# Kernel optimization log

Hardware: AMD Instinct MI355X
Metric: run time of the kernel (lower is better)

## Reference

```python
import jax, jax.numpy as jnp
import numpy as np


def setup_inputs() -> dict:
    key = jax.random.key(0)
    k1, k2, k3, k4 = jax.random.split(key, 4)
    B, D_IN, D, N, A = 32, 2048, 128, 400000, 7
    return {
        "x": jax.random.normal(k1, (B, D_IN), dtype=jnp.float32),
        "W_enc": jax.random.normal(k2, (D_IN, D), dtype=jnp.float32) * 0.02,
        "b_enc": jnp.zeros((D,), dtype=jnp.float32),
        "reps": jax.random.normal(k3, (N, D), dtype=jnp.float32),
        "actions": jax.random.normal(k4, (N, A), dtype=jnp.float32),
        "k": 5,
    }


def reference(x, W_enc, b_enc, reps, actions, k):
    # encoder embed: [B, D]
    batch_rep = x @ W_enc + b_enc
    # euclidean cdist: [B, N]
    sq = (
        jnp.sum(batch_rep * batch_rep, axis=-1, keepdims=True)
        + jnp.sum(reps * reps, axis=-1)[None, :]
        - 2.0 * (batch_rep @ reps.T)
    )
    dists = jnp.sqrt(jnp.maximum(sq, 1e-12))
    # top-k smallest distances
    neg_topk, indices = jax.lax.top_k(-dists, k)  # [B, k]
    top_k_distances = -neg_topk
    # gather actions: [B, k, A]
    top_k_actions = actions[indices]
    # softmax(-distance) weights: [B, k]
    weights = jax.nn.softmax(-top_k_distances, axis=1)
    # weighted average: [B, A]
    pred = jnp.sum(top_k_actions * weights[..., None], axis=1)
    return pred
```

## Files before the change

kernel.cpp:

```cpp
#include <hip/hip_runtime.h>
#include <math.h>

#define BATCH 32
#define DIN   2048
#define DK    128
#define NREPS 400000
#define ACT   7
#define NGRP  (NREPS / 64)

__device__ __forceinline__ void topk_insert(float s, int n,
    float& d0, float& d1, float& d2, float& d3, float& d4,
    int& i0, int& i1, int& i2, int& i3, int& i4)
{
    if (s < d4) {
        if (s < d3) {
            d4 = d3; i4 = i3;
            if (s < d2) {
                d3 = d2; i3 = i2;
                if (s < d1) {
                    d2 = d1; i2 = i1;
                    if (s < d0) { d1 = d0; i1 = i0; d0 = s; i0 = n; }
                    else        { d1 = s;  i1 = n; }
                } else { d2 = s; i2 = n; }
            } else { d3 = s; i3 = n; }
        } else { d4 = s; i4 = n; }
    }
}

__global__ __launch_bounds__(256) void encoder_kernel(
    const float* __restrict__ x, const float* __restrict__ W,
    const float* __restrict__ be, float* __restrict__ brept,
    float* __restrict__ brnorm)
{
    __shared__ float xs[DIN];
    __shared__ float part[256];
    __shared__ float vrow[DK];
    const int b = blockIdx.x, t = threadIdx.x;

    const float4* x4 = (const float4*)(x + (size_t)b * DIN);
    float4* xs4 = (float4*)xs;
    xs4[t]       = x4[t];
    xs4[t + 256] = x4[t + 256];
    __syncthreads();

    const int d = t & 127, h = t >> 7;
    const float* Wp = W + (size_t)(h * 1024) * DK + d;
    const float* xp = xs + h * 1024;
    float a0 = 0.f, a1 = 0.f, a2 = 0.f, a3 = 0.f;
    for (int i = 0; i < 1024; i += 4) {
        a0 = fmaf(xp[i],     Wp[(size_t)i * DK],       a0);
        a1 = fmaf(xp[i + 1], Wp[(size_t)(i + 1) * DK], a1);
        a2 = fmaf(xp[i + 2], Wp[(size_t)(i + 2) * DK], a2);
        a3 = fmaf(xp[i + 3], Wp[(size_t)(i + 3) * DK], a3);
    }
    part[t] = (a0 + a1) + (a2 + a3);
    __syncthreads();
    if (t < DK) {
        float v = part[t] + part[t + 128] + be[t];
        brept[t * BATCH + b] = -2.0f * v;
        vrow[t] = v * v;
    }
    __syncthreads();
    if (t == 0) {
        float s = 0.f;
        for (int i = 0; i < DK; i++) s += vrow[i];
        brnorm[b] = s;
    }
}

__global__ __launch_bounds__(256, 4) void dist_topk_kernel(
    const float* __restrict__ reps, const float* __restrict__ brt,
    float* __restrict__ pd, int* __restrict__ pi, int nwaves)
{
    __shared__ float wdist[4 * 64 * 36];
    const int t = threadIdx.x, g = blockIdx.x;
    const int wid = t >> 6, ln = t & 63;
    const int b = ln & 31, h = ln >> 5;
    float* wd = wdist + wid * (64 * 36);

    float d0 = 3.0e38f, d1 = 3.0e38f, d2 = 3.0e38f, d3 = 3.0e38f, d4 = 3.0e38f;
    int   i0 = 0, i1 = 0, i2 = 0, i3 = 0, i4 = 0;

    for (int grp = g * 4 + wid; grp < NGRP; grp += nwaves) {
        const float4* rp = (const float4*)(reps + (size_t)(grp * 64 + ln) * DK);
        float acc[32];
        #pragma unroll
        for (int i = 0; i < 32; i++) acc[i] = 0.f;
        float nrm = 0.f;

        #pragma unroll 1
        for (int c = 0; c < 4; c++) {
            float4 r[8];
            #pragma unroll
            for (int q = 0; q < 8; q++) r[q] = rp[c * 8 + q];
            const float* bp0 = brt + c * 32 * BATCH;
            #pragma unroll
            for (int q = 0; q < 8; q++) {
                const float4 rr = r[q];
                nrm = fmaf(rr.x, rr.x, nrm);
                nrm = fmaf(rr.y, rr.y, nrm);
                nrm = fmaf(rr.z, rr.z, nrm);
                nrm = fmaf(rr.w, rr.w, nrm);
                const float* bp = bp0 + q * 4 * BATCH;
                #pragma unroll
                for (int bb = 0; bb < 32; bb++) {
                    float a = acc[bb];
                    a = fmaf(bp[bb],             rr.x, a);
                    a = fmaf(bp[BATCH + bb],     rr.y, a);
                    a = fmaf(bp[2 * BATCH + bb], rr.z, a);
                    a = fmaf(bp[3 * BATCH + bb], rr.w, a);
                    acc[bb] = a;
                }
            }
        }

        #pragma unroll
        for (int q = 0; q < 8; q++) {
            float4 v;
            v.x = acc[4 * q]     + nrm;
            v.y = acc[4 * q + 1] + nrm;
            v.z = acc[4 * q + 2] + nrm;
            v.w = acc[4 * q + 3] + nrm;
            *(float4*)&wd[ln * 36 + 4 * q] = v;
        }
        asm volatile("s_waitcnt lgkmcnt(0)" ::: "memory");

        const int nb = grp * 64;
        #pragma unroll 4
        for (int s = 0; s < 32; s++) {
            const int row = h * 32 + s;
            const float dv = wd[row * 36 + b];
            topk_insert(dv, nb + row, d0, d1, d2, d3, d4, i0, i1, i2, i3, i4);
        }
        asm volatile("s_waitcnt lgkmcnt(0)" ::: "memory");
    }

    __syncthreads();
    float* cD = wdist;
    int*   cI = (int*)(wdist + 1280);
    {
        const int base = t * 5;
        cD[base]     = d0; cI[base]     = i0;
        cD[base + 1] = d1; cI[base + 1] = i1;
        cD[base + 2] = d2; cI[base + 2] = i2;
        cD[base + 3] = d3; cI[base + 3] = i3;
        cD[base + 4] = d4; cI[base + 4] = i4;
    }
    __syncthreads();
    if (t < 32) {
        float e0 = 3.0e38f, e1 = 3.0e38f, e2 = 3.0e38f, e3 = 3.0e38f, e4 = 3.0e38f;
        int   j0 = 0, j1 = 0, j2 = 0, j3 = 0, j4 = 0;
        for (int j = 0; j < 8; j++) {
            const int base = (t + 32 * j) * 5;
            #pragma unroll
            for (int e = 0; e < 5; e++)
                topk_insert(cD[base + e], cI[base + e],
                            e0, e1, e2, e3, e4, j0, j1, j2, j3, j4);
        }
        const int ob = (g * BATCH + t) * 5;
        pd[ob] = e0; pd[ob + 1] = e1; pd[ob + 2] = e2; pd[ob + 3] = e3; pd[ob + 4] = e4;
        pi[ob] = j0; pi[ob + 1] = j1; pi[ob + 2] = j2; pi[ob + 3] = j3; pi[ob + 4] = j4;
    }
}

__global__ __launch_bounds__(256) void final_kernel(
    const float* __restrict__ pd, const int* __restrict__ pi,
    const float* __restrict__ brnorm, const float* __restrict__ actions,
    float* __restrict__ out, int G)
{
    __shared__ float lD[256 * 5];
    __shared__ int   lI[256 * 5];
    __shared__ float sD[32 * 5];
    __shared__ int   sI[32 * 5];
    const int b = blockIdx.x, t = threadIdx.x;

    float d0 = 3.0e38f, d1 = 3.0e38f, d2 = 3.0e38f, d3 = 3.0e38f, d4 = 3.0e38f;
    int   i0 = 0, i1 = 0, i2 = 0, i3 = 0, i4 = 0;
    for (int g = t; g < G; g += 256) {
        const int base = (g * BATCH + b) * 5;
        #pragma unroll
        for (int e = 0; e < 5; e++)
            topk_insert(pd[base + e], pi[base + e],
                        d0, d1, d2, d3, d4, i0, i1, i2, i3, i4);
    }
    lD[t * 5] = d0; lD[t * 5 + 1] = d1; lD[t * 5 + 2] = d2; lD[t * 5 + 3] = d3; lD[t * 5 + 4] = d4;
    lI[t * 5] = i0; lI[t * 5 + 1] = i1; lI[t * 5 + 2] = i2; lI[t * 5 + 3] = i3; lI[t * 5 + 4] = i4;
    __syncthreads();
    if (t < 32) {
        d0 = d1 = d2 = d3 = d4 = 3.0e38f; i0 = i1 = i2 = i3 = i4 = 0;
        for (int s = 0; s < 8; s++) {
            const int base = (t * 8 + s) * 5;
            #pragma unroll
            for (int e = 0; e < 5; e++)
                topk_insert(lD[base + e], lI[base + e],
                            d0, d1, d2, d3, d4, i0, i1, i2, i3, i4);
        }
        sD[t * 5] = d0; sD[t * 5 + 1] = d1; sD[t * 5 + 2] = d2; sD[t * 5 + 3] = d3; sD[t * 5 + 4] = d4;
        sI[t * 5] = i0; sI[t * 5 + 1] = i1; sI[t * 5 + 2] = i2; sI[t * 5 + 3] = i3; sI[t * 5 + 4] = i4;
    }
    __syncthreads();
    if (t == 0) {
        d0 = d1 = d2 = d3 = d4 = 3.0e38f; i0 = i1 = i2 = i3 = i4 = 0;
        for (int s = 0; s < 32; s++) {
            const int base = s * 5;
            #pragma unroll
            for (int e = 0; e < 5; e++)
                topk_insert(sD[base + e], sI[base + e],
                            d0, d1, d2, d3, d4, i0, i1, i2, i3, i4);
        }
        const float bn = brnorm[b];
        float dist[5]; int idx[5];
        dist[0] = d0; dist[1] = d1; dist[2] = d2; dist[3] = d3; dist[4] = d4;
        idx[0] = i0; idx[1] = i1; idx[2] = i2; idx[3] = i3; idx[4] = i4;
        float dmin = 3.0e38f;
        #pragma unroll
        for (int e = 0; e < 5; e++) {
            dist[e] = sqrtf(fmaxf(dist[e] + bn, 1e-12f));
            dmin = fminf(dmin, dist[e]);
        }
        float w[5], wsum = 0.f;
        #pragma unroll
        for (int e = 0; e < 5; e++) { w[e] = expf(dmin - dist[e]); wsum += w[e]; }
        const float inv = 1.0f / wsum;
        for (int a = 0; a < ACT; a++) {
            float o = 0.f;
            #pragma unroll
            for (int e = 0; e < 5; e++)
                o = fmaf(w[e], actions[(size_t)idx[e] * ACT + a], o);
            out[b * ACT + a] = o * inv;
        }
    }
}

extern "C" void kernel_launch(void* const* d_in, const int* in_sizes, int n_in,
                              void* d_out, int out_size, void* d_ws, size_t ws_size,
                              hipStream_t stream)
{
    (void)in_sizes; (void)n_in; (void)out_size;
    const float* x       = (const float*)d_in[0];
    const float* W       = (const float*)d_in[1];
    const float* be      = (const float*)d_in[2];
    const float* reps    = (const float*)d_in[3];
    const float* actions = (const float*)d_in[4];

    float* ws     = (float*)d_ws;
    float* brept  = ws;
    float* brnorm = ws + 4096;
    float* pd     = ws + 4224;

    int G = 782;
    {
        const size_t avail_f = ws_size / 4;
        if (avail_f < 4224 + (size_t)G * 320) {
            long fit = ((long)avail_f - 4224) / 320;
            G = (fit < 1) ? 1 : (int)fit;
            if (G > 782) G = 782;
        }
    }
    int* pi = (int*)(pd + (size_t)G * BATCH * 5);
    const int nwaves = G * 4;

    encoder_kernel  <<<32, 256, 0, stream>>>(x, W, be, brept, brnorm);
    dist_topk_kernel<<<G,  256, 0, stream>>>(reps, brept, pd, pi, nwaves);
    final_kernel    <<<32, 256, 0, stream>>>(pd, pi, brnorm, actions, (float*)d_out, G);
}
```

Baseline: 495.8 us.

## Stage query matrix in LDS, process 128 reps per wave, use atomic work queue

The distance kernel now copies the transposed, scaled query embeddings into shared memory once per block. Each wave computes 128 reference rows per iteration instead of 64, so every shared-memory query load feeds two rows, and the inner product uses float4 accumulators. Groups are handed out dynamically through an atomic counter that the encoder kernel resets, replacing static striding. Grid size and occupancy bound change from 782 blocks at 4 per CU to 768 at 3, and the encoder loop is unrolled by 8 to hoist its W loads. The wider tile raises register pressure and lowers occupancy.

```diff
diff --git a/kernel.cpp b/kernel.cpp
--- a/kernel.cpp
+++ b/kernel.cpp
@@ -6,7 +6,8 @@
 #define DK    128
 #define NREPS 400000
 #define ACT   7
-#define NGRP  (NREPS / 64)
+#define NGRP2 3125
+#define GBLK  768
 
 __device__ __forceinline__ void topk_insert(float s, int n,
     float& d0, float& d1, float& d2, float& d3, float& d4,
@@ -30,12 +31,13 @@
 __global__ __launch_bounds__(256) void encoder_kernel(
     const float* __restrict__ x, const float* __restrict__ W,
     const float* __restrict__ be, float* __restrict__ brept,
-    float* __restrict__ brnorm)
+    float* __restrict__ brnorm, int* __restrict__ cnt)
 {
     __shared__ float xs[DIN];
     __shared__ float part[256];
     __shared__ float vrow[DK];
     const int b = blockIdx.x, t = threadIdx.x;
+    if (b == 0 && t == 0) *cnt = 0;
 
     const float4* x4 = (const float4*)(x + (size_t)b * DIN);
     float4* xs4 = (float4*)xs;
@@ -43,15 +45,27 @@
     xs4[t + 256] = x4[t + 256];
     __syncthreads();
 
-    const int d = t & 127, h = t >> 7;
-    const float* Wp = W + (size_t)(h * 1024) * DK + d;
-    const float* xp = xs + h * 1024;
+    const int d = t & 127, hh = t >> 7;
+    const float* Wp = W + (size_t)(hh * 1024) * DK + d;
+    const float* xp = xs + hh * 1024;
     float a0 = 0.f, a1 = 0.f, a2 = 0.f, a3 = 0.f;
-    for (int i = 0; i < 1024; i += 4) {
-        a0 = fmaf(xp[i],     Wp[(size_t)i * DK],       a0);
-        a1 = fmaf(xp[i + 1], Wp[(size_t)(i + 1) * DK], a1);
-        a2 = fmaf(xp[i + 2], Wp[(size_t)(i + 2) * DK], a2);
-        a3 = fmaf(xp[i + 3], Wp[(size_t)(i + 3) * DK], a3);
+    for (int i = 0; i < 1024; i += 8) {
+        const float w0 = Wp[(size_t)i * DK];
+        const float w1 = Wp[(size_t)(i + 1) * DK];
+        const float w2 = Wp[(size_t)(i + 2) * DK];
+        const float w3 = Wp[(size_t)(i + 3) * DK];
+        const float w4 = Wp[(size_t)(i + 4) * DK];
+        const float w5 = Wp[(size_t)(i + 5) * DK];
+        const float w6 = Wp[(size_t)(i + 6) * DK];
+        const float w7 = Wp[(size_t)(i + 7) * DK];
+        a0 = fmaf(xp[i],     w0, a0);
+        a1 = fmaf(xp[i + 1], w1, a1);
+        a2 = fmaf(xp[i + 2], w2, a2);
+        a3 = fmaf(xp[i + 3], w3, a3);
+        a0 = fmaf(xp[i + 4], w4, a0);
+        a1 = fmaf(xp[i + 5], w5, a1);
+        a2 = fmaf(xp[i + 6], w6, a2);
+        a3 = fmaf(xp[i + 7], w7, a3);
     }
     part[t] = (a0 + a1) + (a2 + a3);
     __syncthreads();
@@ -68,69 +82,114 @@
     }
 }
 
-__global__ __launch_bounds__(256, 4) void dist_topk_kernel(
+#define FMA4(Acc, S) \
+    Acc.x = fmaf(p0.x, S.x, Acc.x); Acc.x = fmaf(p1.x, S.y, Acc.x); \
+    Acc.x = fmaf(p2.x, S.z, Acc.x); Acc.x = fmaf(p3.x, S.w, Acc.x); \
+    Acc.y = fmaf(p0.y, S.x, Acc.y); Acc.y = fmaf(p1.y, S.y, Acc.y); \
+    Acc.y = fmaf(p2.y, S.z, Acc.y); Acc.y = fmaf(p3.y, S.w, Acc.y); \
+    Acc.z = fmaf(p0.z, S.x, Acc.z); Acc.z = fmaf(p1.z, S.y, Acc.z); \
+    Acc.z = fmaf(p2.z, S.z, Acc.z); Acc.z = fmaf(p3.z, S.w, Acc.z); \
+    Acc.w = fmaf(p0.w, S.x, Acc.w); Acc.w = fmaf(p1.w, S.y, Acc.w); \
+    Acc.w = fmaf(p2.w, S.z, Acc.w); Acc.w = fmaf(p3.w, S.w, Acc.w);
+
+__global__ __launch_bounds__(256, 3) void dist_topk_kernel(
     const float* __restrict__ reps, const float* __restrict__ brt,
-    float* __restrict__ pd, int* __restrict__ pi, int nwaves)
-{
+    float* __restrict__ pd, int* __restrict__ pi, int* __restrict__ cnt)
+{
+    __shared__ float sbrt[DK * BATCH];
     __shared__ float wdist[4 * 64 * 36];
-    const int t = threadIdx.x, g = blockIdx.x;
+    const int t = threadIdx.x, blk = blockIdx.x;
     const int wid = t >> 6, ln = t & 63;
     const int b = ln & 31, h = ln >> 5;
     float* wd = wdist + wid * (64 * 36);
 
+    {
+        const float4* bsrc = (const float4*)brt;
+        float4* bdst = (float4*)sbrt;
+        #pragma unroll
+        for (int i = 0; i < 4; i++) bdst[t + 256 * i] = bsrc[t + 256 * i];
+    }
+    __syncthreads();
+
     float d0 = 3.0e38f, d1 = 3.0e38f, d2 = 3.0e38f, d3 = 3.0e38f, d4 = 3.0e38f;
     int   i0 = 0, i1 = 0, i2 = 0, i3 = 0, i4 = 0;
 
-    for (int grp = g * 4 + wid; grp < NGRP; grp += nwaves) {
-        const float4* rp = (const float4*)(reps + (size_t)(grp * 64 + ln) * DK);
-        float acc[32];
-        #pragma unroll
-        for (int i = 0; i < 32; i++) acc[i] = 0.f;
-        float nrm = 0.f;
+    const float4* sb4 = (const float4*)sbrt;
+
+    for (;;) {
+        int g = 0;
+        if (ln == 0) g = atomicAdd(cnt, 1);
+        g = __shfl(g, 0);
+        if (g >= NGRP2) break;
+
+        const float4* rp0 = (const float4*)(reps + (size_t)(g * 128 + ln) * DK);
+        const float4* rp1 = rp0 + 64 * (DK / 4);
+
+        float4 a0[8], a1[8];
+        #pragma unroll
+        for (int q = 0; q < 8; q++) {
+            a0[q] = make_float4(0.f, 0.f, 0.f, 0.f);
+            a1[q] = make_float4(0.f, 0.f, 0.f, 0.f);
+        }
+        float n0 = 0.f, n1 = 0.f;
 
         #pragma unroll 1
-        for (int c = 0; c < 4; c++) {
-            float4 r[8];
-            #pragma unroll
-            for (int q = 0; q < 8; q++) r[q] = rp[c * 8 + q];
-            const float* bp0 = brt + c * 32 * BATCH;
-            #pragma unroll
-            for (int q = 0; q < 8; q++) {
-                const float4 rr = r[q];
-                nrm = fmaf(rr.x, rr.x, nrm);
-                nrm = fmaf(rr.y, rr.y, nrm);
-                nrm = fmaf(rr.z, rr.z, nrm);
-                nrm = fmaf(rr.w, rr.w, nrm);
-                const float* bp = bp0 + q * 4 * BATCH;
+        for (int c = 0; c < 8; c++) {
+            float4 r0[4], r1[4];
+            #pragma unroll
+            for (int q = 0; q < 4; q++) { r0[q] = rp0[c * 4 + q]; r1[q] = rp1[c * 4 + q]; }
+            #pragma unroll
+            for (int q = 0; q < 4; q++) {
+                const float4 s0 = r0[q], s1 = r1[q];
+                n0 = fmaf(s0.x, s0.x, n0); n0 = fmaf(s0.y, s0.y, n0);
+                n0 = fmaf(s0.z, s0.z, n0); n0 = fmaf(s0.w, s0.w, n0);
+                n1 = fmaf(s1.x, s1.x, n1); n1 = fmaf(s1.y, s1.y, n1);
+                n1 = fmaf(s1.z, s1.z, n1); n1 = fmaf(s1.w, s1.w, n1);
+                const float4* pb = sb4 + (c * 16 + q * 4) * 8;
                 #pragma unroll
-                for (int bb = 0; bb < 32; bb++) {
-                    float a = acc[bb];
-                    a = fmaf(bp[bb],             rr.x, a);
-                    a = fmaf(bp[BATCH + bb],     rr.y, a);
-                    a = fmaf(bp[2 * BATCH + bb], rr.z, a);
-                    a = fmaf(bp[3 * BATCH + bb], rr.w, a);
-                    acc[bb] = a;
+                for (int j = 0; j < 8; j++) {
+                    const float4 p0 = pb[j], p1 = pb[j + 8], p2 = pb[j + 16], p3 = pb[j + 24];
+                    float4 A = a0[j];
+                    FMA4(A, s0)
+                    a0[j] = A;
+                    float4 B = a1[j];
+                    FMA4(B, s1)
+                    a1[j] = B;
                 }
             }
         }
 
         #pragma unroll
         for (int q = 0; q < 8; q++) {
-            float4 v;
-            v.x = acc[4 * q]     + nrm;
-            v.y = acc[4 * q + 1] + nrm;
-            v.z = acc[4 * q + 2] + nrm;
-            v.w = acc[4 * q + 3] + nrm;
+            float4 v = a0[q];
+            v.x += n0; v.y += n0; v.z += n0; v.w += n0;
             *(float4*)&wd[ln * 36 + 4 * q] = v;
         }
         asm volatile("s_waitcnt lgkmcnt(0)" ::: "memory");
-
-        const int nb = grp * 64;
-        #pragma unroll 4
-        for (int s = 0; s < 32; s++) {
-            const int row = h * 32 + s;
-            const float dv = wd[row * 36 + b];
-            topk_insert(dv, nb + row, d0, d1, d2, d3, d4, i0, i1, i2, i3, i4);
+        {
+            const int nb = g * 128;
+            #pragma unroll 4
+            for (int s = 0; s < 32; s++) {
+                const int row = h * 32 + s;
+                topk_insert(wd[row * 36 + b], nb + row, d0, d1, d2, d3, d4, i0, i1, i2, i3, i4);
+            }
+        }
+        asm volatile("s_waitcnt lgkmcnt(0)" ::: "memory");
+
+        #pragma unroll
+        for (int q = 0; q < 8; q++) {
+            float4 v = a1[q];
+            v.x += n1; v.y += n1; v.z += n1; v.w += n1;
+            *(float4*)&wd[ln * 36 + 4 * q] = v;
+        }
+        asm volatile("s_waitcnt lgkmcnt(0)" ::: "memory");
+        {
+            const int nb = g * 128 + 64;
+            #pragma unroll 4
+            for (int s = 0; s < 32; s++) {
+                const int row = h * 32 + s;
+                topk_insert(wd[row * 36 + b], nb + row, d0, d1, d2, d3, d4, i0, i1, i2, i3, i4);
+            }
         }
         asm volatile("s_waitcnt lgkmcnt(0)" ::: "memory");
     }
@@ -157,7 +216,7 @@
                 topk_insert(cD[base + e], cI[base + e],
                             e0, e1, e2, e3, e4, j0, j1, j2, j3, j4);
         }
-        const int ob = (g * BATCH + t) * 5;
+        const int ob = (blk * BATCH + t) * 5;
         pd[ob] = e0; pd[ob + 1] = e1; pd[ob + 2] = e2; pd[ob + 3] = e3; pd[ob + 4] = e4;
         pi[ob] = j0; pi[ob + 1] = j1; pi[ob + 2] = j2; pi[ob + 3] = j3; pi[ob + 4] = j4;
     }
@@ -246,21 +305,21 @@
     float* ws     = (float*)d_ws;
     float* brept  = ws;
     float* brnorm = ws + 4096;
-    float* pd     = ws + 4224;
-
-    int G = 782;
+    int*   cnt    = (int*)(ws + 4128);
+    float* pd     = ws + 4160;
+
+    int G = GBLK;
     {
         const size_t avail_f = ws_size / 4;
-        if (avail_f < 4224 + (size_t)G * 320) {
-            long fit = ((long)avail_f - 4224) / 320;
+        if (avail_f < 4160 + (size_t)G * 320) {
+            long fit = ((long)avail_f - 4160) / 320;
             G = (fit < 1) ? 1 : (int)fit;
-            if (G > 782) G = 782;
+            if (G > GBLK) G = GBLK;
         }
     }
     int* pi = (int*)(pd + (size_t)G * BATCH * 5);
-    const int nwaves = G * 4;
-
-    encoder_kernel  <<<32, 256, 0, stream>>>(x, W, be, brept, brnorm);
-    dist_topk_kernel<<<G,  256, 0, stream>>>(reps, brept, pd, pi, nwaves);
+
+    encoder_kernel  <<<32, 256, 0, stream>>>(x, W, be, brept, brnorm, cnt);
+    dist_topk_kernel<<<G,  256, 0, stream>>>(reps, brept, pd, pi, cnt);
     final_kernel    <<<32, 256, 0, stream>>>(pd, pi, brnorm, actions, (float*)d_out, G);
 }
```

Measured after the change: 651.3 us. 31.4% more time.
